# Optimization experiments

Hardware: AMD Instinct MI355X
Metric: run time of the kernel (lower is better)

The kernel has to match this reference:

```python
import jax, jax.numpy as jnp
import numpy as np

N = 50000
E = 1600000
DIM = 128
RC = 5.0
DEPTH = 3


def setup_inputs() -> dict:
    key = jax.random.key(0)
    kv, ke, ks, kd, kw, kb, krs, ksig = jax.random.split(key, 8)
    v = jax.random.normal(kv, (N, DIM), dtype=jnp.float32)
    # edge distances in [0, rc]
    e = jax.random.uniform(ke, (E, 1), dtype=jnp.float32) * RC
    src = jax.random.randint(ks, (E,), 0, N, dtype=jnp.int32)
    dst = jax.random.randint(kd, (E,), 0, N, dtype=jnp.int32)
    # learned params: A = nn.Linear(dim, dim); rs, sigma = torch.rand(1)
    A_w = jax.random.normal(kw, (DIM, DIM), dtype=jnp.float32) / np.sqrt(DIM)
    A_b = jax.random.normal(kb, (DIM,), dtype=jnp.float32) * 0.01
    rs = jax.random.uniform(krs, (1,), dtype=jnp.float32)
    sigma = jax.random.uniform(ksig, (1,), dtype=jnp.float32)
    return {"v": v, "e": e, "src": src, "dst": dst,
            "A_w": A_w, "A_b": A_b, "rs": rs, "sigma": sigma}


def _edge_envelope(r, rs, sigma):
    # exp(-(r-rs)^2/sigma^2) * 0.5 * cos(pi*r/rc) * (r < rc)
    gauss = jnp.exp(-jnp.square(r - rs) / jnp.square(sigma))
    cutoff = 0.5 * jnp.cos(np.pi * r / RC) * (r < RC).astype(r.dtype)
    return gauss * cutoff


def reference(v, e, src, dst, A_w, A_b, rs, sigma):
    f = _edge_envelope(e, rs, sigma)  # [E, 1]
    cur = v
    for _ in range(DEPTH):
        msg = f * cur[src]  # gather src node feats, weight by edge envelope: [E, DIM]
        svf = jax.ops.segment_sum(msg, dst, num_segments=N)  # scatter-sum to dst: [N, DIM]
        cur = jax.nn.relu((svf + v) @ A_w.T + A_b)  # linear + relu, skip from original v
    return cur
```

## Files before the change

kernel.cpp:

```cpp
#include <hip/hip_runtime.h>
#include <math.h>

#define N_NODES 50000
#define N_PAD   50048
#define N_EDGES 1600000
#define DIM     128
#define RCUT    5.0f
#define NGROUP  (N_PAD / 64)
#define NB_PRE  512
#define CH_PRE  (N_EDGES / NB_PRE)

typedef __attribute__((ext_vector_type(8))) __bf16 bf16x8;
typedef __attribute__((ext_vector_type(4))) float  f32x4;

__device__ __forceinline__ float bf_lo(unsigned int u) { return __uint_as_float(u << 16); }
__device__ __forceinline__ float bf_hi(unsigned int u) { return __uint_as_float(u & 0xffff0000u); }
__device__ __forceinline__ unsigned short f2bf(float x) {
    unsigned int u = __float_as_uint(x);
    u += 0x7fffu + ((u >> 16) & 1u);
    return (unsigned short)(u >> 16);
}

__global__ void convert_v_kernel(const float* __restrict__ v,
                                 unsigned short* __restrict__ vb) {
    int i = blockIdx.x * blockDim.x + threadIdx.x;
    if (i >= N_NODES * DIM / 4) return;
    float4 x = ((const float4*)v)[i];
    uint2 o;
    o.x = (unsigned)f2bf(x.x) | ((unsigned)f2bf(x.y) << 16);
    o.y = (unsigned)f2bf(x.z) | ((unsigned)f2bf(x.w) << 16);
    ((uint2*)vb)[i] = o;
}

__global__ void wprep_kernel(const float* __restrict__ Aw, uint4* __restrict__ wfrag) {
    int t = blockIdx.x * 256 + threadIdx.x;
    if (t >= 2048) return;
    int lane = t & 63, nt = (t >> 6) & 7, kk = t >> 9;
    int n  = nt * 16 + (lane & 15);
    int k0 = kk * 32 + (lane >> 4) * 8;
    unsigned short h[8];
    #pragma unroll
    for (int i = 0; i < 8; ++i) h[i] = f2bf(Aw[n * DIM + k0 + i]);
    uint4 o;
    o.x = h[0] | ((unsigned)h[1] << 16); o.y = h[2] | ((unsigned)h[3] << 16);
    o.z = h[4] | ((unsigned)h[5] << 16); o.w = h[6] | ((unsigned)h[7] << 16);
    wfrag[t] = o;
}

__global__ __launch_bounds__(256) void countp_kernel(const int* __restrict__ dst,
                                                     int* __restrict__ partial) {
    __shared__ int h[NGROUP];
    int b = blockIdx.x, tid = threadIdx.x;
    for (int g = tid; g < NGROUP; g += 256) h[g] = 0;
    __syncthreads();
    int beg = b * CH_PRE, end = beg + CH_PRE;
    for (int i = beg + tid; i < end; i += 256)
        atomicAdd(&h[dst[i] >> 6], 1);
    __syncthreads();
    for (int g = tid; g < NGROUP; g += 256) partial[b * NGROUP + g] = h[g];
}

__global__ __launch_bounds__(256) void sumA_kernel(const int* __restrict__ partial,
                                                   int* __restrict__ gtot) {
    __shared__ int red[256];
    int g = blockIdx.x, tid = threadIdx.x;
    int s = partial[tid * NGROUP + g] + partial[(tid + 256) * NGROUP + g];
    red[tid] = s; __syncthreads();
    for (int d = 128; d > 0; d >>= 1) { if (tid < d) red[tid] += red[tid + d]; __syncthreads(); }
    if (tid == 0) gtot[g] = red[0];
}

__global__ __launch_bounds__(256) void scanB_kernel(const int* __restrict__ gtot,
                                                    int* __restrict__ goff) {
    __shared__ int part[256];
    int tid = threadIdx.x;
    int i0 = tid * 4;
    int v[4]; int s = 0;
    #pragma unroll
    for (int k = 0; k < 4; ++k) { int i = i0 + k; v[k] = (i < NGROUP) ? gtot[i] : 0; s += v[k]; }
    part[tid] = s; __syncthreads();
    for (int d = 1; d < 256; d <<= 1) {
        int val = (tid >= d) ? part[tid - d] : 0;
        __syncthreads(); part[tid] += val; __syncthreads();
    }
    int run = (tid == 0) ? 0 : part[tid - 1];
    #pragma unroll
    for (int k = 0; k < 4; ++k) {
        int i = i0 + k;
        if (i < NGROUP) { goff[i] = run; run += v[k]; }
    }
    if (tid == 0) goff[NGROUP] = N_EDGES;
}

__global__ __launch_bounds__(256) void scanC_kernel(const int* __restrict__ partial,
                                                    const int* __restrict__ goff,
                                                    int* __restrict__ pbase) {
    __shared__ int part[256];
    int g = blockIdx.x, tid = threadIdx.x;
    int v0 = partial[(2 * tid) * NGROUP + g];
    int v1 = partial[(2 * tid + 1) * NGROUP + g];
    part[tid] = v0 + v1; __syncthreads();
    for (int d = 1; d < 256; d <<= 1) {
        int val = (tid >= d) ? part[tid - d] : 0;
        __syncthreads(); part[tid] += val; __syncthreads();
    }
    int run = goff[g] + ((tid == 0) ? 0 : part[tid - 1]);
    pbase[(2 * tid) * NGROUP + g] = run;
    pbase[(2 * tid + 1) * NGROUP + g] = run + v0;
}

__global__ __launch_bounds__(256) void reorder_kernel(
        const float* __restrict__ e,
        const int*   __restrict__ src,
        const int*   __restrict__ dst,
        const float* __restrict__ rs,
        const float* __restrict__ sigma,
        const int*   __restrict__ pbase,
        int2* __restrict__ metaT) {
    __shared__ int base[NGROUP];
    __shared__ int cnt[NGROUP];
    int b = blockIdx.x, tid = threadIdx.x;
    for (int g = tid; g < NGROUP; g += 256) { base[g] = pbase[b * NGROUP + g]; cnt[g] = 0; }
    __syncthreads();
    float rsv = rs[0], sg = sigma[0];
    int beg = b * CH_PRE, end = beg + CH_PRE;
    for (int i = beg + tid; i < end; i += 256) {
        float r  = e[i];
        float d  = r - rsv;
        float gauss = expf(-(d * d) / (sg * sg));
        float cut   = 0.5f * cosf(r * (float)(M_PI / (double)RCUT));
        cut = (r < RCUT) ? cut : 0.0f;
        float fe = gauss * cut;
        int dn  = dst[i];
        int g   = dn >> 6;
        int lr  = atomicAdd(&cnt[g], 1);
        int slot = base[g] + lr;
        metaT[slot] = make_int2(src[i] * (DIM * 2) | ((dn & 63) << 24),
                                __float_as_int(fe));
    }
}

__global__ __launch_bounds__(256) void tagsort_kernel(
        const int2* __restrict__ metaT,
        const int*  __restrict__ goff,
        int2* __restrict__ meta,
        int*  __restrict__ off) {
    __shared__ int cnt[64], base[64], cur[64];
    int g = blockIdx.x, tid = threadIdx.x;
    int sbeg = goff[g], send = goff[g + 1];
    if (tid < 64) cnt[tid] = 0;
    __syncthreads();
    for (int i = sbeg + tid; i < send; i += 256)
        atomicAdd(&cnt[(metaT[i].x >> 24) & 63], 1);
    __syncthreads();
    if (tid == 0) {
        int run = 0;
        #pragma unroll
        for (int t = 0; t < 64; ++t) { base[t] = run; cur[t] = run; run += cnt[t]; }
    }
    __syncthreads();
    if (tid < 64) {
        int node = g * 64 + tid;
        if (node <= N_NODES) off[node] = sbeg + base[tid];
    }
    __syncthreads();
    for (int i = sbeg + tid; i < send; i += 256) {
        int2 m = metaT[i];
        int tag = (m.x >> 24) & 63;
        int lr = atomicAdd(&cur[tag], 1);
        meta[sbeg + lr] = make_int2(m.x & 0x00FFFFFF, m.y);
    }
}

__global__ __launch_bounds__(256) void gather_kernel(
        const unsigned short* __restrict__ cur,
        const float* __restrict__ v,
        const int2*  __restrict__ meta,
        const int*   __restrict__ off,
        unsigned short* __restrict__ svf) {
    int n    = (blockIdx.x << 2) + (threadIdx.x >> 6);
    int lane = threadIdx.x & 63;
    if (n >= N_NODES) return;

    float2 vv = *(const float2*)(v + (size_t)n * DIM + lane * 2);
    float a0 = vv.x, a1 = vv.y;

    int beg = __builtin_amdgcn_readfirstlane(off[n]);
    int end = __builtin_amdgcn_readfirstlane(off[n + 1]);
    const char* base = (const char*)cur + lane * 4;

    int c = beg;
    if ((c & 1) && c < end) {
        int2 m = meta[c];
        unsigned r = *(const unsigned*)(base + (unsigned)m.x);
        float f = __int_as_float(m.y);
        a0 = fmaf(f, bf_lo(r), a0); a1 = fmaf(f, bf_hi(r), a1);
        ++c;
    }
    for (; c + 8 <= end; c += 8) {
        int4 m0 = *(const int4*)(meta + c);
        int4 m1 = *(const int4*)(meta + c + 2);
        int4 m2 = *(const int4*)(meta + c + 4);
        int4 m3 = *(const int4*)(meta + c + 6);
        unsigned r0 = *(const unsigned*)(base + (unsigned)m0.x);
        unsigned r1 = *(const unsigned*)(base + (unsigned)m0.z);
        unsigned r2 = *(const unsigned*)(base + (unsigned)m1.x);
        unsigned r3 = *(const unsigned*)(base + (unsigned)m1.z);
        unsigned r4 = *(const unsigned*)(base + (unsigned)m2.x);
        unsigned r5 = *(const unsigned*)(base + (unsigned)m2.z);
        unsigned r6 = *(const unsigned*)(base + (unsigned)m3.x);
        unsigned r7 = *(const unsigned*)(base + (unsigned)m3.z);
        float f0 = __int_as_float(m0.y), f1 = __int_as_float(m0.w);
        float f2 = __int_as_float(m1.y), f3 = __int_as_float(m1.w);
        float f4 = __int_as_float(m2.y), f5 = __int_as_float(m2.w);
        float f6 = __int_as_float(m3.y), f7 = __int_as_float(m3.w);
        a0 = fmaf(f0, bf_lo(r0), a0); a1 = fmaf(f0, bf_hi(r0), a1);
        a0 = fmaf(f1, bf_lo(r1), a0); a1 = fmaf(f1, bf_hi(r1), a1);
        a0 = fmaf(f2, bf_lo(r2), a0); a1 = fmaf(f2, bf_hi(r2), a1);
        a0 = fmaf(f3, bf_lo(r3), a0); a1 = fmaf(f3, bf_hi(r3), a1);
        a0 = fmaf(f4, bf_lo(r4), a0); a1 = fmaf(f4, bf_hi(r4), a1);
        a0 = fmaf(f5, bf_lo(r5), a0); a1 = fmaf(f5, bf_hi(r5), a1);
        a0 = fmaf(f6, bf_lo(r6), a0); a1 = fmaf(f6, bf_hi(r6), a1);
        a0 = fmaf(f7, bf_lo(r7), a0); a1 = fmaf(f7, bf_hi(r7), a1);
    }
    for (; c < end; ++c) {
        int2 m = meta[c];
        unsigned r = *(const unsigned*)(base + (unsigned)m.x);
        float f = __int_as_float(m.y);
        a0 = fmaf(f, bf_lo(r), a0); a1 = fmaf(f, bf_hi(r), a1);
    }
    unsigned o = (unsigned)f2bf(a0) | ((unsigned)f2bf(a1) << 16);
    *(unsigned*)(svf + (size_t)n * DIM + lane * 2) = o;
}

__global__ __launch_bounds__(256) void gemm_kernel(
        const unsigned short* __restrict__ X,
        const uint4* __restrict__ wfrag,
        const float* __restrict__ bias,
        unsigned short* __restrict__ out_bf,
        float* __restrict__ out_f,
        int last) {
    __shared__ uint4 wlds[2048];
    int tid = threadIdx.x;
    for (int i = tid; i < 2048; i += 256) wlds[i] = wfrag[i];

    int wv = tid >> 6, lane = tid & 63;
    int quad = lane >> 4, l16 = lane & 15;
    int row = blockIdx.x * 64 + wv * 16 + l16;

    f32x4 acc[8];
    #pragma unroll
    for (int i = 0; i < 8; ++i) acc[i] = (f32x4){0.f, 0.f, 0.f, 0.f};

    __syncthreads();

    const unsigned short* xp = X + (size_t)row * DIM + quad * 8;
    #pragma unroll
    for (int kk = 0; kk < 4; ++kk) {
        bf16x8 af = *(const bf16x8*)(xp + kk * 32);
        #pragma unroll
        for (int nt = 0; nt < 8; ++nt) {
            uint4 w = wlds[(kk * 8 + nt) * 64 + lane];
            bf16x8 bfr = __builtin_bit_cast(bf16x8, w);
            acc[nt] = __builtin_amdgcn_mfma_f32_16x16x32_bf16(af, bfr, acc[nt], 0, 0, 0);
        }
    }

    int orow0 = blockIdx.x * 64 + wv * 16 + quad * 4;
    #pragma unroll
    for (int nt = 0; nt < 8; ++nt) {
        int col = nt * 16 + l16;
        float b = bias[col];
        #pragma unroll
        for (int r = 0; r < 4; ++r) {
            int orow = orow0 + r;
            if (orow < N_NODES) {
                float val = fmaxf(acc[nt][r] + b, 0.f);
                if (last) out_f[(size_t)orow * DIM + col] = val;
                else      out_bf[(size_t)orow * DIM + col] = f2bf(val);
            }
        }
    }
}

extern "C" void kernel_launch(void* const* d_in, const int* in_sizes, int n_in,
                              void* d_out, int out_size, void* d_ws, size_t ws_size,
                              hipStream_t stream) {
    const float* v     = (const float*)d_in[0];
    const float* e     = (const float*)d_in[1];
    const int*   src   = (const int*)  d_in[2];
    const int*   dst   = (const int*)  d_in[3];
    const float* Aw    = (const float*)d_in[4];
    const float* Ab    = (const float*)d_in[5];
    const float* rs    = (const float*)d_in[6];
    const float* sigma = (const float*)d_in[7];
    float* out = (float*)d_out;

    char* p = (char*)d_ws;
    int2*           meta  = (int2*)p;            p += (size_t)N_EDGES * 8;
    unsigned short* bufV  = (unsigned short*)p;  p += (size_t)N_PAD * DIM * 2;
    unsigned short* bufA  = (unsigned short*)p;  p += (size_t)N_PAD * DIM * 2;
    unsigned short* bufB  = (unsigned short*)p;  p += (size_t)N_PAD * DIM * 2;
    uint4*          wfrag = (uint4*)p;           p += 2048 * 16;
    int*            off   = (int*)p;             p += (size_t)(N_NODES + 1) * 4;
    int*            gtot  = (int*)p;             p += (NGROUP + 2) * 4;
    int*            goff  = (int*)p;             p += (NGROUP + 2) * 4;
    int2* metaT   = (int2*)bufA;
    int*  partial = (int*)bufB;
    int*  pbase   = partial + NB_PRE * NGROUP;

    convert_v_kernel<<<(N_NODES * DIM / 4 + 255) / 256, 256, 0, stream>>>(v, bufV);
    wprep_kernel<<<8, 256, 0, stream>>>(Aw, wfrag);
    countp_kernel<<<NB_PRE, 256, 0, stream>>>(dst, partial);
    sumA_kernel<<<NGROUP, 256, 0, stream>>>(partial, gtot);
    scanB_kernel<<<1, 256, 0, stream>>>(gtot, goff);
    scanC_kernel<<<NGROUP, 256, 0, stream>>>(partial, goff, pbase);
    reorder_kernel<<<NB_PRE, 256, 0, stream>>>(e, src, dst, rs, sigma, pbase, metaT);
    tagsort_kernel<<<NGROUP, 256, 0, stream>>>(metaT, goff, meta, off);

    const int GB = (N_NODES + 3) / 4;
    const int MB = N_PAD / 64;

    gather_kernel<<<GB, 256, 0, stream>>>(bufV, v, meta, off, bufA);
    gemm_kernel<<<MB, 256, 0, stream>>>(bufA, wfrag, Ab, bufB, nullptr, 0);
    gather_kernel<<<GB, 256, 0, stream>>>(bufB, v, meta, off, bufA);
    gemm_kernel<<<MB, 256, 0, stream>>>(bufA, wfrag, Ab, bufV, nullptr, 0);
    gather_kernel<<<GB, 256, 0, stream>>>(bufV, v, meta, off, bufA);
    gemm_kernel<<<MB, 256, 0, stream>>>(bufA, wfrag, Ab, nullptr, out, 1);
}
```

Before: 365.4 us.

## Fuse gather and GEMM per layer, merge prep kernels, simplify preprocessing scans

Merges the per-layer gather and GEMM into one 1024-thread kernel: 16 waves each gather one node row into LDS, then 8 waves run MFMA against weight fragments read straight from global memory. This removes the bf16 svf round-trip and three launches. It also fuses the v-conversion and weight-prep kernels, cuts the preprocessing partition count to 128 with simple per-group serial sum and base kernels, and widens the gather unroll to 16 edges. The skip term now adds the bf16-rounded v instead of fp32 v, which costs some accuracy. The GEMM now uses only 16 rows per block with no weight reuse in LDS, which risks poor MFMA efficiency.

New measurement: 423.3 us. +15.8%, slower.

```diff
diff --git a/kernel.cpp b/kernel.cpp
--- a/kernel.cpp
+++ b/kernel.cpp
@@ -7,7 +7,7 @@
 #define DIM     128
 #define RCUT    5.0f
 #define NGROUP  (N_PAD / 64)
-#define NB_PRE  512
+#define NB_PRE  128
 #define CH_PRE  (N_EDGES / NB_PRE)
 
 typedef __attribute__((ext_vector_type(8))) __bf16 bf16x8;
@@ -21,30 +21,30 @@
     return (unsigned short)(u >> 16);
 }
 
-__global__ void convert_v_kernel(const float* __restrict__ v,
-                                 unsigned short* __restrict__ vb) {
-    int i = blockIdx.x * blockDim.x + threadIdx.x;
-    if (i >= N_NODES * DIM / 4) return;
-    float4 x = ((const float4*)v)[i];
-    uint2 o;
-    o.x = (unsigned)f2bf(x.x) | ((unsigned)f2bf(x.y) << 16);
-    o.y = (unsigned)f2bf(x.z) | ((unsigned)f2bf(x.w) << 16);
-    ((uint2*)vb)[i] = o;
-}
-
-__global__ void wprep_kernel(const float* __restrict__ Aw, uint4* __restrict__ wfrag) {
-    int t = blockIdx.x * 256 + threadIdx.x;
-    if (t >= 2048) return;
-    int lane = t & 63, nt = (t >> 6) & 7, kk = t >> 9;
-    int n  = nt * 16 + (lane & 15);
-    int k0 = kk * 32 + (lane >> 4) * 8;
-    unsigned short h[8];
-    #pragma unroll
-    for (int i = 0; i < 8; ++i) h[i] = f2bf(Aw[n * DIM + k0 + i]);
-    uint4 o;
-    o.x = h[0] | ((unsigned)h[1] << 16); o.y = h[2] | ((unsigned)h[3] << 16);
-    o.z = h[4] | ((unsigned)h[5] << 16); o.w = h[6] | ((unsigned)h[7] << 16);
-    wfrag[t] = o;
+__global__ __launch_bounds__(256) void prep_kernel(
+        const float* __restrict__ v, unsigned short* __restrict__ vb,
+        const float* __restrict__ Aw, uint4* __restrict__ wfrag) {
+    int b = blockIdx.x;
+    if (b < 6250) {
+        int i = b * 256 + threadIdx.x;
+        float4 x = ((const float4*)v)[i];
+        uint2 o;
+        o.x = (unsigned)f2bf(x.x) | ((unsigned)f2bf(x.y) << 16);
+        o.y = (unsigned)f2bf(x.z) | ((unsigned)f2bf(x.w) << 16);
+        ((uint2*)vb)[i] = o;
+    } else {
+        int t = (b - 6250) * 256 + threadIdx.x;
+        int lane = t & 63, nt = (t >> 6) & 7, kk = t >> 9;
+        int n  = nt * 16 + (lane & 15);
+        int k0 = kk * 32 + (lane >> 4) * 8;
+        unsigned short h[8];
+        #pragma unroll
+        for (int i = 0; i < 8; ++i) h[i] = f2bf(Aw[n * DIM + k0 + i]);
+        uint4 o;
+        o.x = h[0] | ((unsigned)h[1] << 16); o.y = h[2] | ((unsigned)h[3] << 16);
+        o.z = h[4] | ((unsigned)h[5] << 16); o.w = h[6] | ((unsigned)h[7] << 16);
+        wfrag[t] = o;
+    }
 }
 
 __global__ __launch_bounds__(256) void countp_kernel(const int* __restrict__ dst,
@@ -60,17 +60,16 @@
     for (int g = tid; g < NGROUP; g += 256) partial[b * NGROUP + g] = h[g];
 }
 
-__global__ __launch_bounds__(256) void sumA_kernel(const int* __restrict__ partial,
+__global__ __launch_bounds__(256) void ktot_kernel(const int* __restrict__ partial,
                                                    int* __restrict__ gtot) {
-    __shared__ int red[256];
-    int g = blockIdx.x, tid = threadIdx.x;
-    int s = partial[tid * NGROUP + g] + partial[(tid + 256) * NGROUP + g];
-    red[tid] = s; __syncthreads();
-    for (int d = 128; d > 0; d >>= 1) { if (tid < d) red[tid] += red[tid + d]; __syncthreads(); }
-    if (tid == 0) gtot[g] = red[0];
-}
-
-__global__ __launch_bounds__(256) void scanB_kernel(const int* __restrict__ gtot,
+    int g = blockIdx.x * 256 + threadIdx.x;
+    if (g >= NGROUP) return;
+    int s = 0;
+    for (int b = 0; b < NB_PRE; ++b) s += partial[b * NGROUP + g];
+    gtot[g] = s;
+}
+
+__global__ __launch_bounds__(256) void kscan_kernel(const int* __restrict__ gtot,
                                                     int* __restrict__ goff) {
     __shared__ int part[256];
     int tid = threadIdx.x;
@@ -92,21 +91,16 @@
     if (tid == 0) goff[NGROUP] = N_EDGES;
 }
 
-__global__ __launch_bounds__(256) void scanC_kernel(const int* __restrict__ partial,
+__global__ __launch_bounds__(256) void kbase_kernel(const int* __restrict__ partial,
                                                     const int* __restrict__ goff,
                                                     int* __restrict__ pbase) {
-    __shared__ int part[256];
-    int g = blockIdx.x, tid = threadIdx.x;
-    int v0 = partial[(2 * tid) * NGROUP + g];
-    int v1 = partial[(2 * tid + 1) * NGROUP + g];
-    part[tid] = v0 + v1; __syncthreads();
-    for (int d = 1; d < 256; d <<= 1) {
-        int val = (tid >= d) ? part[tid - d] : 0;
-        __syncthreads(); part[tid] += val; __syncthreads();
-    }
-    int run = goff[g] + ((tid == 0) ? 0 : part[tid - 1]);
-    pbase[(2 * tid) * NGROUP + g] = run;
-    pbase[(2 * tid + 1) * NGROUP + g] = run + v0;
+    int g = blockIdx.x * 256 + threadIdx.x;
+    if (g >= NGROUP) return;
+    int run = goff[g];
+    for (int b = 0; b < NB_PRE; ++b) {
+        pbase[b * NGROUP + g] = run;
+        run += partial[b * NGROUP + g];
+    }
 }
 
 __global__ __launch_bounds__(256) void reorder_kernel(
@@ -131,12 +125,11 @@
         float cut   = 0.5f * cosf(r * (float)(M_PI / (double)RCUT));
         cut = (r < RCUT) ? cut : 0.0f;
         float fe = gauss * cut;
-        int dn  = dst[i];
-        int g   = dn >> 6;
-        int lr  = atomicAdd(&cnt[g], 1);
-        int slot = base[g] + lr;
-        metaT[slot] = make_int2(src[i] * (DIM * 2) | ((dn & 63) << 24),
-                                __float_as_int(fe));
+        int dn = dst[i];
+        int g  = dn >> 6;
+        int lr = atomicAdd(&cnt[g], 1);
+        metaT[base[g] + lr] = make_int2(src[i] * (DIM * 2) | ((dn & 63) << 24),
+                                        __float_as_int(fe));
     }
 }
 
@@ -172,32 +165,79 @@
     }
 }
 
-__global__ __launch_bounds__(256) void gather_kernel(
+#define EDGE2(mx, mf, rr)                                        \
+    do {                                                         \
+        float ff = __int_as_float(mf);                           \
+        a0 = fmaf(ff, bf_lo(rr), a0);                            \
+        a1 = fmaf(ff, bf_hi(rr), a1);                            \
+    } while (0)
+
+__global__ __launch_bounds__(1024) void layer_kernel(
         const unsigned short* __restrict__ cur,
-        const float* __restrict__ v,
+        const unsigned short* __restrict__ vb,
         const int2*  __restrict__ meta,
         const int*   __restrict__ off,
-        unsigned short* __restrict__ svf) {
-    int n    = (blockIdx.x << 2) + (threadIdx.x >> 6);
-    int lane = threadIdx.x & 63;
-    if (n >= N_NODES) return;
-
-    float2 vv = *(const float2*)(v + (size_t)n * DIM + lane * 2);
-    float a0 = vv.x, a1 = vv.y;
-
-    int beg = __builtin_amdgcn_readfirstlane(off[n]);
-    int end = __builtin_amdgcn_readfirstlane(off[n + 1]);
+        const uint4* __restrict__ wfrag,
+        const float* __restrict__ bias,
+        unsigned short* __restrict__ out_bf,
+        float* __restrict__ out_f,
+        int last) {
+    __shared__ __align__(16) unsigned short xs[16 * 144];
+
+    int tid  = threadIdx.x;
+    int wv   = tid >> 6, lane = tid & 63;
+    int n    = blockIdx.x * 16 + wv;
+
+    float a0 = 0.f, a1 = 0.f;
+    int beg = 0, end = 0;
+    if (n < N_NODES) {
+        beg = __builtin_amdgcn_readfirstlane(off[n]);
+        end = __builtin_amdgcn_readfirstlane(off[n + 1]);
+    }
     const char* base = (const char*)cur + lane * 4;
 
     int c = beg;
     if ((c & 1) && c < end) {
         int2 m = meta[c];
-        unsigned r = *(const unsigned*)(base + (unsigned)m.x);
-        float f = __int_as_float(m.y);
-        a0 = fmaf(f, bf_lo(r), a0); a1 = fmaf(f, bf_hi(r), a1);
+        unsigned rr = *(const unsigned*)(base + (unsigned)m.x);
+        EDGE2(m.x, m.y, rr);
         ++c;
     }
-    for (; c + 8 <= end; c += 8) {
+    for (; c + 16 <= end; c += 16) {
+        int4 m0 = *(const int4*)(meta + c);
+        int4 m1 = *(const int4*)(meta + c + 2);
+        int4 m2 = *(const int4*)(meta + c + 4);
+        int4 m3 = *(const int4*)(meta + c + 6);
+        int4 m4 = *(const int4*)(meta + c + 8);
+        int4 m5 = *(const int4*)(meta + c + 10);
+        int4 m6 = *(const int4*)(meta + c + 12);
+        int4 m7 = *(const int4*)(meta + c + 14);
+        unsigned r0  = *(const unsigned*)(base + (unsigned)m0.x);
+        unsigned r1  = *(const unsigned*)(base + (unsigned)m0.z);
+        unsigned r2  = *(const unsigned*)(base + (unsigned)m1.x);
+        unsigned r3  = *(const unsigned*)(base + (unsigned)m1.z);
+        unsigned r4  = *(const unsigned*)(base + (unsigned)m2.x);
+        unsigned r5  = *(const unsigned*)(base + (unsigned)m2.z);
+        unsigned r6  = *(const unsigned*)(base + (unsigned)m3.x);
+        unsigned r7  = *(const unsigned*)(base + (unsigned)m3.z);
+        unsigned r8  = *(const unsigned*)(base + (unsigned)m4.x);
+        unsigned r9  = *(const unsigned*)(base + (unsigned)m4.z);
+        unsigned r10 = *(const unsigned*)(base + (unsigned)m5.x);
+        unsigned r11 = *(const unsigned*)(base + (unsigned)m5.z);
+        unsigned r12 = *(const unsigned*)(base + (unsigned)m6.x);
+        unsigned r13 = *(const unsigned*)(base + (unsigned)m6.z);
+        unsigned r14 = *(const unsigned*)(base + (unsigned)m7.x);
+        unsigned r15 = *(const unsigned*)(base + (unsigned)m7.z);
+        EDGE2(m0.x, m0.y, r0);  EDGE2(m0.z, m0.w, r1);
+        EDGE2(m1.x, m1.y, r2);  EDGE2(m1.z, m1.w, r3);
+        EDGE2(m2.x, m2.y, r4);  EDGE2(m2.z, m2.w, r5);
+        EDGE2(m3.x, m3.y, r6);  EDGE2(m3.z, m3.w, r7);
+        EDGE2(m4.x, m4.y, r8);  EDGE2(m4.z, m4.w, r9);
+        EDGE2(m5.x, m5.y, r10); EDGE2(m5.z, m5.w, r11);
+        EDGE2(m6.x, m6.y, r12); EDGE2(m6.z, m6.w, r13);
+        EDGE2(m7.x, m7.y, r14); EDGE2(m7.z, m7.w, r15);
+    }
+    if (c + 8 <= end) {
         int4 m0 = *(const int4*)(meta + c);
         int4 m1 = *(const int4*)(meta + c + 2);
         int4 m2 = *(const int4*)(meta + c + 4);
@@ -210,72 +250,43 @@
         unsigned r5 = *(const unsigned*)(base + (unsigned)m2.z);
         unsigned r6 = *(const unsigned*)(base + (unsigned)m3.x);
         unsigned r7 = *(const unsigned*)(base + (unsigned)m3.z);
-        float f0 = __int_as_float(m0.y), f1 = __int_as_float(m0.w);
-        float f2 = __int_as_float(m1.y), f3 = __int_as_float(m1.w);
-        float f4 = __int_as_float(m2.y), f5 = __int_as_float(m2.w);
-        float f6 = __int_as_float(m3.y), f7 = __int_as_float(m3.w);
-        a0 = fmaf(f0, bf_lo(r0), a0); a1 = fmaf(f0, bf_hi(r0), a1);
-        a0 = fmaf(f1, bf_lo(r1), a0); a1 = fmaf(f1, bf_hi(r1), a1);
-        a0 = fmaf(f2, bf_lo(r2), a0); a1 = fmaf(f2, bf_hi(r2), a1);
-        a0 = fmaf(f3, bf_lo(r3), a0); a1 = fmaf(f3, bf_hi(r3), a1);
-        a0 = fmaf(f4, bf_lo(r4), a0); a1 = fmaf(f4, bf_hi(r4), a1);
-        a0 = fmaf(f5, bf_lo(r5), a0); a1 = fmaf(f5, bf_hi(r5), a1);
-        a0 = fmaf(f6, bf_lo(r6), a0); a1 = fmaf(f6, bf_hi(r6), a1);
-        a0 = fmaf(f7, bf_lo(r7), a0); a1 = fmaf(f7, bf_hi(r7), a1);
+        EDGE2(m0.x, m0.y, r0); EDGE2(m0.z, m0.w, r1);
+        EDGE2(m1.x, m1.y, r2); EDGE2(m1.z, m1.w, r3);
+        EDGE2(m2.x, m2.y, r4); EDGE2(m2.z, m2.w, r5);
+        EDGE2(m3.x, m3.y, r6); EDGE2(m3.z, m3.w, r7);
+        c += 8;
     }
     for (; c < end; ++c) {
         int2 m = meta[c];
-        unsigned r = *(const unsigned*)(base + (unsigned)m.x);
-        float f = __int_as_float(m.y);
-        a0 = fmaf(f, bf_lo(r), a0); a1 = fmaf(f, bf_hi(r), a1);
-    }
-    unsigned o = (unsigned)f2bf(a0) | ((unsigned)f2bf(a1) << 16);
-    *(unsigned*)(svf + (size_t)n * DIM + lane * 2) = o;
-}
-
-__global__ __launch_bounds__(256) void gemm_kernel(
-        const unsigned short* __restrict__ X,
-        const uint4* __restrict__ wfrag,
-        const float* __restrict__ bias,
-        unsigned short* __restrict__ out_bf,
-        float* __restrict__ out_f,
-        int last) {
-    __shared__ uint4 wlds[2048];
-    int tid = threadIdx.x;
-    for (int i = tid; i < 2048; i += 256) wlds[i] = wfrag[i];
-
-    int wv = tid >> 6, lane = tid & 63;
-    int quad = lane >> 4, l16 = lane & 15;
-    int row = blockIdx.x * 64 + wv * 16 + l16;
-
-    f32x4 acc[8];
-    #pragma unroll
-    for (int i = 0; i < 8; ++i) acc[i] = (f32x4){0.f, 0.f, 0.f, 0.f};
-
-    __syncthreads();
-
-    const unsigned short* xp = X + (size_t)row * DIM + quad * 8;
-    #pragma unroll
-    for (int kk = 0; kk < 4; ++kk) {
-        bf16x8 af = *(const bf16x8*)(xp + kk * 32);
+        unsigned rr = *(const unsigned*)(base + (unsigned)m.x);
+        EDGE2(m.x, m.y, rr);
+    }
+
+    if (n < N_NODES) {
+        unsigned rr = *(const unsigned*)((const char*)vb + (size_t)n * (DIM * 2) + lane * 4);
+        a0 += bf_lo(rr); a1 += bf_hi(rr);
+    }
+    *(unsigned*)&xs[wv * 144 + lane * 2] =
+        (unsigned)f2bf(a0) | ((unsigned)f2bf(a1) << 16);
+    __syncthreads();
+
+    if (wv < 8) {
+        int quad = lane >> 4, l16 = lane & 15;
+        f32x4 acc = {0.f, 0.f, 0.f, 0.f};
         #pragma unroll
-        for (int nt = 0; nt < 8; ++nt) {
-            uint4 w = wlds[(kk * 8 + nt) * 64 + lane];
-            bf16x8 bfr = __builtin_bit_cast(bf16x8, w);
-            acc[nt] = __builtin_amdgcn_mfma_f32_16x16x32_bf16(af, bfr, acc[nt], 0, 0, 0);
+        for (int kk = 0; kk < 4; ++kk) {
+            bf16x8 af = *(const bf16x8*)&xs[l16 * 144 + kk * 32 + quad * 8];
+            uint4 w = wfrag[(kk * 8 + wv) * 64 + lane];
+            acc = __builtin_amdgcn_mfma_f32_16x16x32_bf16(af, __builtin_bit_cast(bf16x8, w), acc, 0, 0, 0);
         }
-    }
-
-    int orow0 = blockIdx.x * 64 + wv * 16 + quad * 4;
-    #pragma unroll
-    for (int nt = 0; nt < 8; ++nt) {
-        int col = nt * 16 + l16;
+        int rbase = blockIdx.x * 16 + quad * 4;
+        int col = wv * 16 + l16;
         float b = bias[col];
         #pragma unroll
         for (int r = 0; r < 4; ++r) {
-            int orow = orow0 + r;
+            int orow = rbase + r;
             if (orow < N_NODES) {
-                float val = fmaxf(acc[nt][r] + b, 0.f);
+                float val = fmaxf(acc[r] + b, 0.f);
                 if (last) out_f[(size_t)orow * DIM + col] = val;
                 else      out_bf[(size_t)orow * DIM + col] = f2bf(val);
             }
@@ -309,22 +320,16 @@
     int*  partial = (int*)bufB;
     int*  pbase   = partial + NB_PRE * NGROUP;
 
-    convert_v_kernel<<<(N_NODES * DIM / 4 + 255) / 256, 256, 0, stream>>>(v, bufV);
-    wprep_kernel<<<8, 256, 0, stream>>>(Aw, wfrag);
+    prep_kernel<<<6258, 256, 0, stream>>>(v, bufV, Aw, wfrag);
     countp_kernel<<<NB_PRE, 256, 0, stream>>>(dst, partial);
-    sumA_kernel<<<NGROUP, 256, 0, stream>>>(partial, gtot);
-    scanB_kernel<<<1, 256, 0, stream>>>(gtot, goff);
-    scanC_kernel<<<NGROUP, 256, 0, stream>>>(partial, goff, pbase);
+    ktot_kernel<<<(NGROUP + 255) / 256, 256, 0, stream>>>(partial, gtot);
+    kscan_kernel<<<1, 256, 0, stream>>>(gtot, goff);
+    kbase_kernel<<<(NGROUP + 255) / 256, 256, 0, stream>>>(partial, goff, pbase);
     reorder_kernel<<<NB_PRE, 256, 0, stream>>>(e, src, dst, rs, sigma, pbase, metaT);
     tagsort_kernel<<<NGROUP, 256, 0, stream>>>(metaT, goff, meta, off);
 
-    const int GB = (N_NODES + 3) / 4;
-    const int MB = N_PAD / 64;
-
-    gather_kernel<<<GB, 256, 0, stream>>>(bufV, v, meta, off, bufA);
-    gemm_kernel<<<MB, 256, 0, stream>>>(bufA, wfrag, Ab, bufB, nullptr, 0);
-    gather_kernel<<<GB, 256, 0, stream>>>(bufB, v, meta, off, bufA);
-    gemm_kernel<<<MB, 256, 0, stream>>>(bufA, wfrag, Ab, bufV, nullptr, 0);
-    gather_kernel<<<GB, 256, 0, stream>>>(bufV, v, meta, off, bufA);
-    gemm_kernel<<<MB, 256, 0, stream>>>(bufA, wfrag, Ab, nullptr, out, 1);
-}
+    const int LB = N_PAD / 16;
+    layer_kernel<<<LB, 1024, 0, stream>>>(bufV, bufV, meta, off, wfrag, Ab, bufA, nullptr, 0);
+    layer_kernel<<<LB, 1024, 0, stream>>>(bufA, bufV, meta, off, wfrag, Ab, bufB, nullptr, 0);
+    layer_kernel<<<LB, 1024, 0, stream>>>(bufB, bufV, meta, off, wfrag, Ab, nullptr, out, 1);
+}
```
